# Kernel optimization log

Measured on AMD Instinct MI355X. Metric: run time of the kernel, lower is better.

The kernel has to match this reference:

```python
import jax, jax.numpy as jnp
import numpy as np
from jax import lax

B, S, D, H = 256, 1024, 64, 128


def setup_inputs() -> dict:
    key = jax.random.key(0)
    ks = jax.random.split(key, 11)
    s_in = 1.0 / np.sqrt(H)  # torch RNNCell/Linear init scale (uniform bound); normal scale ok for testing
    return {
        "inputs": jax.random.normal(ks[0], (B, S, D), jnp.float32),
        "Wih_fw": jax.random.normal(ks[1], (H, D), jnp.float32) * s_in,
        "Whh_fw": jax.random.normal(ks[2], (H, H), jnp.float32) * s_in,
        "bih_fw": jax.random.normal(ks[3], (H,), jnp.float32) * s_in,
        "bhh_fw": jax.random.normal(ks[4], (H,), jnp.float32) * s_in,
        "Wih_bw": jax.random.normal(ks[5], (H, D), jnp.float32) * s_in,
        "Whh_bw": jax.random.normal(ks[6], (H, H), jnp.float32) * s_in,
        "bih_bw": jax.random.normal(ks[7], (H,), jnp.float32) * s_in,
        "bhh_bw": jax.random.normal(ks[8], (H,), jnp.float32) * s_in,
        "fc_W": jax.random.normal(ks[9], (1, 2 * H), jnp.float32) * (1.0 / np.sqrt(2 * H)),
        "fc_b": jnp.zeros((1,), jnp.float32),
    }


def _run_dir(inputs, Wih, Whh, bih, bhh, reverse):
    # Precompute input projection for all timesteps: [B,S,H]
    xp = jnp.einsum('bsd,hd->bsh', inputs, Wih) + bih + bhh
    WhhT = Whh.T

    def step(h, x_t):  # x_t: [B,H]
        h_new = jnp.tanh(x_t + h @ WhhT)
        return h_new, h_new

    h0 = jnp.zeros((inputs.shape[0], Whh.shape[0]), inputs.dtype)
    # scan over time; reverse=True processes t = S-1..0 and emits outputs in
    # original time order, matching torch's output_bw[::-1] stacking.
    _, ys = lax.scan(step, h0, jnp.swapaxes(xp, 0, 1), reverse=reverse)
    return jnp.swapaxes(ys, 0, 1)  # [B,S,H]


def reference(inputs, Wih_fw, Whh_fw, bih_fw, bhh_fw,
              Wih_bw, Whh_bw, bih_bw, bhh_bw, fc_W, fc_b):
    out_fw = _run_dir(inputs, Wih_fw, Whh_fw, bih_fw, bhh_fw, reverse=False)
    out_bw = _run_dir(inputs, Wih_bw, Whh_bw, bih_bw, bhh_bw, reverse=True)
    outputs = jnp.concatenate([out_fw, out_bw], axis=2)  # [B,S,2H]
    outputs = outputs @ fc_W.T + fc_b  # [B,S,1]
    return jnp.squeeze(outputs, -1)  # [B,S]
```

## Files before the change

### kernel.cpp

```cpp
#include <hip/hip_runtime.h>

namespace {

constexpr int kS = 1024;
constexpr int kD = 64;
constexpr int kH = 128;

typedef __attribute__((ext_vector_type(2))) _Float16 half2v;
typedef __attribute__((ext_vector_type(4))) float f32x4;
typedef __attribute__((ext_vector_type(8))) _Float16 half8;

__device__ __forceinline__ float fdot2(unsigned w, unsigned h, float acc) {
#if __has_builtin(__builtin_amdgcn_fdot2)
  return __builtin_amdgcn_fdot2(__builtin_bit_cast(half2v, w),
                                __builtin_bit_cast(half2v, h), acc, false);
#else
  float d;
  asm("v_dot2_f32_f16 %0, %1, %2, %3" : "=v"(d) : "v"(w), "v"(h), "v"(acc));
  return d;
#endif
}

__device__ __forceinline__ unsigned rdlane(unsigned v, int k) {
#if __has_builtin(__builtin_amdgcn_readlane)
  return (unsigned)__builtin_amdgcn_readlane((int)v, k);
#else
  return (unsigned)__shfl((int)v, k, 64);
#endif
}

__device__ __forceinline__ unsigned pk16(float a, float b) {
  half2v h;
  h.x = (_Float16)a;
  h.y = (_Float16)b;
  return __builtin_bit_cast(unsigned, h);
}

__device__ __forceinline__ float fast_tanh(float x) {
  x = fminf(fmaxf(x, -15.f), 15.f);
  float e = __expf(2.f * x);
  return (e - 1.f) * __builtin_amdgcn_rcpf(e + 1.f);
}

#if __has_builtin(__builtin_amdgcn_mov_dpp)
__device__ __forceinline__ float lane_xor1(float v) {
  return __int_as_float(__builtin_amdgcn_mov_dpp(__float_as_int(v), 0xB1, 0xF, 0xF, true));
}
#else
__device__ __forceinline__ float lane_xor1(float v) {
  return __int_as_float(__builtin_amdgcn_ds_swizzle(__float_as_int(v), 0x041F));
}
#endif

__device__ __forceinline__ void stage_chunk(const char* g, unsigned* lds, int L) {
#pragma unroll
  for (int k = 0; k < 8; ++k) {
    __builtin_amdgcn_global_load_lds(
        (const __attribute__((address_space(1))) void*)(g + k * 1024 + L * 16),
        (__attribute__((address_space(3))) void*)(lds + k * 256), 16, 0, 0);
  }
}


__global__ __launch_bounds__(256, 2) void xproj_kernel(
    const float* __restrict__ inputs,
    const float* __restrict__ Wih_fw, const float* __restrict__ bih_fw,
    const float* __restrict__ bhh_fw,
    const float* __restrict__ Wih_bw, const float* __restrict__ bih_bw,
    const float* __restrict__ bhh_bw,
    _Float16* __restrict__ xp) {
  __shared__ _Float16 Wl[256 * 80];
  __shared__ _Float16 xl[128 * 80];
  __shared__ float biasl[256];

  const int tid = threadIdx.x;
  const int b = blockIdx.x;
  const int w = tid >> 6;
  const int lane = tid & 63;
  const int n16 = lane & 15;
  const int q = lane >> 4;

  {
    const int jd = tid;
    const float* src = (jd < kH) ? (Wih_fw + jd * kD) : (Wih_bw + (jd - kH) * kD);
    const float4* s4 = (const float4*)src;
#pragma unroll
    for (int k = 0; k < 8; ++k) {
      float4 a = s4[2 * k], c = s4[2 * k + 1];
      half8 h;
      h[0] = (_Float16)a.x; h[1] = (_Float16)a.y; h[2] = (_Float16)a.z; h[3] = (_Float16)a.w;
      h[4] = (_Float16)c.x; h[5] = (_Float16)c.y; h[6] = (_Float16)c.z; h[7] = (_Float16)c.w;
      *(half8*)&Wl[jd * 80 + k * 8] = h;
    }
    biasl[jd] = (jd < kH) ? (bih_fw[jd] + bhh_fw[jd])
                          : (bih_bw[jd - kH] + bhh_bw[jd - kH]);
  }

  for (int ch = 0; ch < 8; ++ch) {
    __syncthreads();
    {
      const int tl = tid >> 1, hf = tid & 1;
      const float4* s4 = (const float4*)(inputs +
          ((size_t)b * kS + ch * 128 + tl) * kD + hf * 32);
#pragma unroll
      for (int k = 0; k < 4; ++k) {
        float4 a = s4[2 * k], c = s4[2 * k + 1];
        half8 h;
        h[0] = (_Float16)a.x; h[1] = (_Float16)a.y; h[2] = (_Float16)a.z; h[3] = (_Float16)a.w;
        h[4] = (_Float16)c.x; h[5] = (_Float16)c.y; h[6] = (_Float16)c.z; h[7] = (_Float16)c.w;
        *(half8*)&xl[tl * 80 + hf * 32 + k * 8] = h;
      }
    }
    __syncthreads();

    half8 bf0[4], bf1[4];
    float bs[4];
#pragma unroll
    for (int nn = 0; nn < 4; ++nn) {
      const int jd = (w * 4 + nn) * 16 + n16;
      bf0[nn] = *(const half8*)&Wl[jd * 80 + q * 8];
      bf1[nn] = *(const half8*)&Wl[jd * 80 + q * 8 + 32];
      bs[nn] = biasl[jd];
    }

#pragma unroll 2
    for (int m = 0; m < 8; ++m) {
      const int trow = m * 16 + n16;
      const half8 a0 = *(const half8*)&xl[trow * 80 + q * 8];
      const half8 a1 = *(const half8*)&xl[trow * 80 + q * 8 + 32];
#pragma unroll
      for (int nn = 0; nn < 4; ++nn) {
        f32x4 acc = {0.f, 0.f, 0.f, 0.f};
        acc = __builtin_amdgcn_mfma_f32_16x16x32_f16(a0, bf0[nn], acc, 0, 0, 0);
        acc = __builtin_amdgcn_mfma_f32_16x16x32_f16(a1, bf1[nn], acc, 0, 0, 0);
        const int jd = (w * 4 + nn) * 16 + n16;
        const int dir = jd >> 7, j = jd & 127;
        const size_t slab = (size_t)(dir * 256 + b) * (kS * kH);
#pragma unroll
        for (int r = 0; r < 4; ++r) {
          const int t = ch * 128 + m * 16 + q * 4 + r;
          const int tt = dir ? (kS - 1 - t) : t;
          xp[slab + (size_t)(tt >> 5) * (32 * kH) + (tt & 31) * kH + j] =
              (_Float16)(acc[r] + bs[nn]);
        }
      }
    }
  }
}

__global__ __launch_bounds__(64, 1) void birnn_step_kernel(
    const _Float16* __restrict__ xp,
    const float* __restrict__ Whh_fw, const float* __restrict__ Whh_bw,
    const float* __restrict__ fcW, const float* __restrict__ fcb,
    float* __restrict__ out) {
  const int dir = blockIdx.x >> 8;
  const int b = blockIdx.x & 255;
  const int L = threadIdx.x;

  __shared__ unsigned jrn[32 * 68];
  __shared__ unsigned xbuf[2][2048];
  __shared__ unsigned fcwl[64];
  __shared__ float outbuf[kS];

  const float* __restrict__ Whh = dir ? Whh_bw : Whh_fw;

  unsigned w0[64], w1[64];
  {
    const float* r0 = Whh + (size_t)(2 * L) * kH;
    const float* r1 = Whh + (size_t)(2 * L + 1) * kH;
#pragma unroll
    for (int k = 0; k < 64; ++k) {
      w0[k] = pk16(r0[2 * k], r0[2 * k + 1]);
      w1[k] = pk16(r1[2 * k], r1[2 * k + 1]);
    }
  }
  fcwl[L] = pk16(fcW[dir * kH + 2 * L], fcW[dir * kH + 2 * L + 1]);

  unsigned hcur = 0;

  const char* slab = (const char*)(xp + (size_t)(dir * 256 + b) * (kS * kH));
  stage_chunk(slab, &xbuf[0][0], L);
  stage_chunk(slab + 8192, &xbuf[1][0], L);
  asm volatile("s_waitcnt vmcnt(0)" ::: "memory");

  for (int c = 0; c < 32; ++c) {
    const unsigned* xb = &xbuf[c & 1][0];

#pragma unroll 2
    for (int s = 0; s < 32; ++s) {
      const unsigned xdw = xb[s * 64 + L];
      float a0 = 0.f, a1 = 0.f, a2 = 0.f, a3 = 0.f;
      float c0 = 0.f, c1 = 0.f, c2 = 0.f, c3 = 0.f;
#pragma unroll
      for (int g = 0; g < 16; ++g) {
        const unsigned h0 = rdlane(hcur, 4 * g + 0);
        const unsigned h1 = rdlane(hcur, 4 * g + 1);
        const unsigned h2 = rdlane(hcur, 4 * g + 2);
        const unsigned h3 = rdlane(hcur, 4 * g + 3);
        a0 = fdot2(w0[4 * g + 0], h0, a0);
        c0 = fdot2(w1[4 * g + 0], h0, c0);
        a1 = fdot2(w0[4 * g + 1], h1, a1);
        c1 = fdot2(w1[4 * g + 1], h1, c1);
        a2 = fdot2(w0[4 * g + 2], h2, a2);
        c2 = fdot2(w1[4 * g + 2], h2, c2);
        a3 = fdot2(w0[4 * g + 3], h3, a3);
        c3 = fdot2(w1[4 * g + 3], h3, c3);
      }
      const half2v xh = __builtin_bit_cast(half2v, xdw);
      const float va = ((a0 + a1) + (a2 + a3)) + (float)xh.x;
      const float vb = ((c0 + c1) + (c2 + c3)) + (float)xh.y;
      hcur = pk16(fast_tanh(va), fast_tanh(vb));
      jrn[s * 68 + L] = hcur;
    }

    {
      const int tl = L >> 1, jh = L & 1;
      const uint4* rp = (const uint4*)&jrn[tl * 68 + jh * 32];
      const uint4* fp = (const uint4*)&fcwl[jh * 32];
      float acc = 0.f;
#pragma unroll
      for (int k = 0; k < 8; ++k) {
        const uint4 hv = rp[k];
        const uint4 fw = fp[k];
        acc = fdot2(fw.x, hv.x, acc);
        acc = fdot2(fw.y, hv.y, acc);
        acc = fdot2(fw.z, hv.z, acc);
        acc = fdot2(fw.w, hv.w, acc);
      }
      acc += lane_xor1(acc);
      if (jh == 0) outbuf[c * 32 + tl] = acc;
    }

    if (c < 30) {
      stage_chunk(slab + (size_t)(c + 2) * 8192, &xbuf[c & 1][0], L);
      asm volatile("s_waitcnt vmcnt(8)" ::: "memory");
    } else if (c == 30) {
      asm volatile("s_waitcnt vmcnt(0)" ::: "memory");
    }
  }

  const float fcb0 = (dir == 0) ? fcb[0] : 0.f;
#pragma unroll
  for (int k = 0; k < 16; ++k) {
    const int t = L + 64 * k;
    const int td = dir ? (kS - 1 - t) : t;
    atomicAdd(&out[(size_t)b * kS + td], outbuf[t] + fcb0);
  }
}

}

extern "C" void kernel_launch(void* const* d_in, const int* in_sizes, int n_in,
                              void* d_out, int out_size, void* d_ws, size_t ws_size,
                              hipStream_t stream) {
  (void)in_sizes; (void)n_in; (void)ws_size;
  const float* inputs = (const float*)d_in[0];
  const float* Wih_fw = (const float*)d_in[1];
  const float* Whh_fw = (const float*)d_in[2];
  const float* bih_fw = (const float*)d_in[3];
  const float* bhh_fw = (const float*)d_in[4];
  const float* Wih_bw = (const float*)d_in[5];
  const float* Whh_bw = (const float*)d_in[6];
  const float* bih_bw = (const float*)d_in[7];
  const float* bhh_bw = (const float*)d_in[8];
  const float* fc_W   = (const float*)d_in[9];
  const float* fc_b   = (const float*)d_in[10];
  float* out = (float*)d_out;
  _Float16* xpw = (_Float16*)d_ws;

  hipMemsetAsync(out, 0, (size_t)out_size * sizeof(float), stream);

  hipLaunchKernelGGL(xproj_kernel, dim3(256), dim3(256), 0, stream,
                     inputs, Wih_fw, bih_fw, bhh_fw, Wih_bw, bih_bw, bhh_bw, xpw);
  hipLaunchKernelGGL(birnn_step_kernel, dim3(512), dim3(64), 0, stream,
                     xpw, Whh_fw, Whh_bw, fc_W, fc_b, out);
}
```

Baseline: 583.3 us.

## Split recurrent step across two waves with LDS exchange of hidden halves

The per-sequence recurrence now runs on two wavefronts instead of one. Each lane computes a single hidden unit and keeps half of its Whh row for its own half of the state and half for the other wave's half. The own half arrives through readlane and the other half through LDS, with a barrier every timestep. Staging of the input projection and the output FC reduction are split between the waves, and their partial sums are combined before the atomics. This halves per-lane dot-product work on the serial critical path, but adds a workgroup barrier and an LDS round trip on every step.

```diff
diff --git a/kernel.cpp b/kernel.cpp
--- a/kernel.cpp
+++ b/kernel.cpp
@@ -52,12 +52,17 @@
 }
 #endif
 
-__device__ __forceinline__ void stage_chunk(const char* g, unsigned* lds, int L) {
-#pragma unroll
-  for (int k = 0; k < 8; ++k) {
+__device__ __forceinline__ void wave_sync() {
+  asm volatile("s_waitcnt lgkmcnt(0)\n\ts_barrier" ::: "memory");
+}
+
+__device__ __forceinline__ void stage_half(const char* g, unsigned* lds, int L, int w) {
+#pragma unroll
+  for (int k = 0; k < 4; ++k) {
+    const int kk = 4 * w + k;
     __builtin_amdgcn_global_load_lds(
-        (const __attribute__((address_space(1))) void*)(g + k * 1024 + L * 16),
-        (__attribute__((address_space(3))) void*)(lds + k * 256), 16, 0, 0);
+        (const __attribute__((address_space(1))) void*)(g + kk * 1024 + L * 16),
+        (__attribute__((address_space(3))) void*)(lds + kk * 256), 16, 0, 0);
   }
 }
 
@@ -148,103 +153,122 @@
   }
 }
 
-__global__ __launch_bounds__(64, 1) void birnn_step_kernel(
+__global__ __launch_bounds__(128, 1) void birnn_step_kernel(
     const _Float16* __restrict__ xp,
     const float* __restrict__ Whh_fw, const float* __restrict__ Whh_bw,
     const float* __restrict__ fcW, const float* __restrict__ fcb,
     float* __restrict__ out) {
   const int dir = blockIdx.x >> 8;
   const int b = blockIdx.x & 255;
-  const int L = threadIdx.x;
+  const int tid = threadIdx.x;
+  const int w = tid >> 6;
+  const int L = tid & 63;
 
   __shared__ unsigned jrn[32 * 68];
   __shared__ unsigned xbuf[2][2048];
   __shared__ unsigned fcwl[64];
-  __shared__ float outbuf[kS];
+  __shared__ float outw[2][kS];
 
   const float* __restrict__ Whh = dir ? Whh_bw : Whh_fw;
 
-  unsigned w0[64], w1[64];
+  unsigned wOwn[32], wOth[32];
   {
-    const float* r0 = Whh + (size_t)(2 * L) * kH;
-    const float* r1 = Whh + (size_t)(2 * L + 1) * kH;
-#pragma unroll
-    for (int k = 0; k < 64; ++k) {
-      w0[k] = pk16(r0[2 * k], r0[2 * k + 1]);
-      w1[k] = pk16(r1[2 * k], r1[2 * k + 1]);
-    }
-  }
-  fcwl[L] = pk16(fcW[dir * kH + 2 * L], fcW[dir * kH + 2 * L + 1]);
-
-  unsigned hcur = 0;
+    const float* r = Whh + (size_t)(64 * w + L) * kH;
+    const int own = 64 * w, oth = 64 * (1 - w);
+#pragma unroll
+    for (int m = 0; m < 32; ++m) {
+      wOwn[m] = pk16(r[own + 2 * m], r[own + 2 * m + 1]);
+      wOth[m] = pk16(r[oth + 2 * m], r[oth + 2 * m + 1]);
+    }
+  }
+  if (w == 0) fcwl[L] = pk16(fcW[dir * kH + 2 * L], fcW[dir * kH + 2 * L + 1]);
+  jrn[31 * 68 + L] = 0;
+
+  unsigned hp_prev = 0;
 
   const char* slab = (const char*)(xp + (size_t)(dir * 256 + b) * (kS * kH));
-  stage_chunk(slab, &xbuf[0][0], L);
-  stage_chunk(slab + 8192, &xbuf[1][0], L);
-  asm volatile("s_waitcnt vmcnt(0)" ::: "memory");
+  stage_half(slab, &xbuf[0][0], L, w);
+  stage_half(slab + 8192, &xbuf[1][0], L, w);
+  asm volatile("s_waitcnt vmcnt(4)" ::: "memory");
 
   for (int c = 0; c < 32; ++c) {
-    const unsigned* xb = &xbuf[c & 1][0];
+    const unsigned short* xs = (const unsigned short*)&xbuf[c & 1][0];
 
 #pragma unroll 2
     for (int s = 0; s < 32; ++s) {
-      const unsigned xdw = xb[s * 64 + L];
-      float a0 = 0.f, a1 = 0.f, a2 = 0.f, a3 = 0.f;
-      float c0 = 0.f, c1 = 0.f, c2 = 0.f, c3 = 0.f;
-#pragma unroll
-      for (int g = 0; g < 16; ++g) {
-        const unsigned h0 = rdlane(hcur, 4 * g + 0);
-        const unsigned h1 = rdlane(hcur, 4 * g + 1);
-        const unsigned h2 = rdlane(hcur, 4 * g + 2);
-        const unsigned h3 = rdlane(hcur, 4 * g + 3);
-        a0 = fdot2(w0[4 * g + 0], h0, a0);
-        c0 = fdot2(w1[4 * g + 0], h0, c0);
-        a1 = fdot2(w0[4 * g + 1], h1, a1);
-        c1 = fdot2(w1[4 * g + 1], h1, c1);
-        a2 = fdot2(w0[4 * g + 2], h2, a2);
-        c2 = fdot2(w1[4 * g + 2], h2, c2);
-        a3 = fdot2(w0[4 * g + 3], h3, a3);
-        c3 = fdot2(w1[4 * g + 3], h3, c3);
+      wave_sync();
+      const int prev = (s + 31) & 31;
+      const uint4* hr = (const uint4*)&jrn[prev * 68 + 32 * (1 - w)];
+      uint4 hv[8];
+#pragma unroll
+      for (int g = 0; g < 8; ++g) hv[g] = hr[g];
+      const unsigned short xraw = xs[s * 128 + 64 * w + L];
+
+      float o0 = 0.f, o1 = 0.f, o2 = 0.f, o3 = 0.f;
+      float t0 = 0.f, t1 = 0.f, t2 = 0.f, t3 = 0.f;
+#pragma unroll
+      for (int g = 0; g < 8; ++g) {
+        const unsigned h0 = rdlane(hp_prev, 8 * g + 0);
+        const unsigned h1 = rdlane(hp_prev, 8 * g + 2);
+        const unsigned h2 = rdlane(hp_prev, 8 * g + 4);
+        const unsigned h3 = rdlane(hp_prev, 8 * g + 6);
+        o0 = fdot2(wOwn[4 * g + 0], h0, o0);
+        t0 = fdot2(wOth[4 * g + 0], hv[g].x, t0);
+        o1 = fdot2(wOwn[4 * g + 1], h1, o1);
+        t1 = fdot2(wOth[4 * g + 1], hv[g].y, t1);
+        o2 = fdot2(wOwn[4 * g + 2], h2, o2);
+        t2 = fdot2(wOth[4 * g + 2], hv[g].z, t2);
+        o3 = fdot2(wOwn[4 * g + 3], h3, o3);
+        t3 = fdot2(wOth[4 * g + 3], hv[g].w, t3);
       }
-      const half2v xh = __builtin_bit_cast(half2v, xdw);
-      const float va = ((a0 + a1) + (a2 + a3)) + (float)xh.x;
-      const float vb = ((c0 + c1) + (c2 + c3)) + (float)xh.y;
-      hcur = pk16(fast_tanh(va), fast_tanh(vb));
-      jrn[s * 68 + L] = hcur;
-    }
+      const float xval = (float)__builtin_bit_cast(_Float16, xraw);
+      const float v = (((o0 + o1) + (o2 + o3)) + ((t0 + t1) + (t2 + t3))) + xval;
+      const float h = fast_tanh(v);
+      const float nb = lane_xor1(h);
+      const float lo = (L & 1) ? nb : h;
+      const float hi = (L & 1) ? h : nb;
+      const unsigned hp = pk16(lo, hi);
+      jrn[s * 68 + 32 * w + (L >> 1)] = hp;
+      hp_prev = hp;
+    }
+
+    wave_sync();
+
+    if (c < 30) stage_half(slab + (size_t)(c + 2) * 8192, &xbuf[c & 1][0], L, w);
 
     {
       const int tl = L >> 1, jh = L & 1;
-      const uint4* rp = (const uint4*)&jrn[tl * 68 + jh * 32];
-      const uint4* fp = (const uint4*)&fcwl[jh * 32];
+      const uint4* rp = (const uint4*)&jrn[tl * 68 + 32 * w + jh * 16];
+      const uint4* fp = (const uint4*)&fcwl[32 * w + jh * 16];
       float acc = 0.f;
 #pragma unroll
-      for (int k = 0; k < 8; ++k) {
-        const uint4 hv = rp[k];
-        const uint4 fw = fp[k];
-        acc = fdot2(fw.x, hv.x, acc);
-        acc = fdot2(fw.y, hv.y, acc);
-        acc = fdot2(fw.z, hv.z, acc);
-        acc = fdot2(fw.w, hv.w, acc);
+      for (int k = 0; k < 4; ++k) {
+        const uint4 hv4 = rp[k];
+        const uint4 fw4 = fp[k];
+        acc = fdot2(fw4.x, hv4.x, acc);
+        acc = fdot2(fw4.y, hv4.y, acc);
+        acc = fdot2(fw4.z, hv4.z, acc);
+        acc = fdot2(fw4.w, hv4.w, acc);
       }
       acc += lane_xor1(acc);
-      if (jh == 0) outbuf[c * 32 + tl] = acc;
+      if (jh == 0) outw[w][c * 32 + tl] = acc;
     }
 
     if (c < 30) {
-      stage_chunk(slab + (size_t)(c + 2) * 8192, &xbuf[c & 1][0], L);
-      asm volatile("s_waitcnt vmcnt(8)" ::: "memory");
+      asm volatile("s_waitcnt vmcnt(4)" ::: "memory");
     } else if (c == 30) {
       asm volatile("s_waitcnt vmcnt(0)" ::: "memory");
     }
   }
 
+  __syncthreads();
+
   const float fcb0 = (dir == 0) ? fcb[0] : 0.f;
 #pragma unroll
-  for (int k = 0; k < 16; ++k) {
-    const int t = L + 64 * k;
+  for (int k = 0; k < 8; ++k) {
+    const int t = k * 128 + tid;
     const int td = dir ? (kS - 1 - t) : t;
-    atomicAdd(&out[(size_t)b * kS + td], outbuf[t] + fcb0);
+    atomicAdd(&out[(size_t)b * kS + td], outw[0][t] + outw[1][t] + fcb0);
   }
 }
 
@@ -272,6 +296,6 @@
 
   hipLaunchKernelGGL(xproj_kernel, dim3(256), dim3(256), 0, stream,
                      inputs, Wih_fw, bih_fw, bhh_fw, Wih_bw, bih_bw, bhh_bw, xpw);
-  hipLaunchKernelGGL(birnn_step_kernel, dim3(512), dim3(64), 0, stream,
+  hipLaunchKernelGGL(birnn_step_kernel, dim3(512), dim3(128), 0, stream,
                      xpw, Whh_fw, Whh_bw, fc_W, fc_b, out);
 }
```

Measured after the change: 720.9 us. +23.6%, slower.
